# Performance work log

Measured on AMD Instinct MI355X. Metric: run time of the kernel, lower is better.

The kernel has to match this reference:

```python
import jax, jax.numpy as jnp
import numpy as np

B, T, D, H = 8, 1024, 1024, 16
DH = D // H
EPS = 1e-5


def setup_inputs() -> dict:
    key = jax.random.key(0)
    ks = jax.random.split(key, 8)
    s = 0.02
    return {
        "x": jax.random.normal(ks[0], (B, T, D), dtype=jnp.float32),
        # per-head Q/K/V weights stacked: (H, in_c, d_head), applied as x @ W
        "Wq": jax.random.normal(ks[1], (H, D, DH), dtype=jnp.float32) * s,
        "Wk": jax.random.normal(ks[2], (H, D, DH), dtype=jnp.float32) * s,
        "Wv": jax.random.normal(ks[3], (H, D, DH), dtype=jnp.float32) * s,
        # FFN weights stored (in, out): y = x @ W
        "W1": jax.random.normal(ks[4], (D, D), dtype=jnp.float32) * s,
        "W2": jax.random.normal(ks[5], (D, D), dtype=jnp.float32) * s,
        "g1": jnp.ones((D,), jnp.float32),
        "b1": jnp.zeros((D,), jnp.float32),
        "g2": jnp.ones((D,), jnp.float32),
        "b2": jnp.zeros((D,), jnp.float32),
    }


def _layer_norm(x, g, b):
    m = jnp.mean(x, axis=-1, keepdims=True)
    v = jnp.mean((x - m) ** 2, axis=-1, keepdims=True)  # biased, as torch LN
    return (x - m) * jax.lax.rsqrt(v + EPS) * g + b


def reference(x, Wq, Wk, Wv, W1, W2, g1, b1, g2, b2):
    b, t, d = x.shape
    dh = Wq.shape[-1]
    q = jnp.einsum("btc,hcd->bhtd", x, Wq)
    k = jnp.einsum("btc,hcd->bhtd", x, Wk)
    v = jnp.einsum("btc,hcd->bhtd", x, Wv)
    attn = jnp.einsum("bhtd,bhsd->bhts", q, k) / (dh ** 0.5)
    # Original: attn @ ones(T,T) -> every column equals rowsum(attn);
    # softmax(dim=1) over the query axis is then constant across columns,
    # so out[t] = softmax_t(rowsum)[t] * sum_s v[s]. Same math, reduced.
    rowsum = attn.sum(axis=-1)               # (B,H,T)
    p = jax.nn.softmax(rowsum, axis=-1)      # softmax over query index t
    vsum = v.sum(axis=2)                     # (B,H,DH)
    head_out = p[..., None] * vsum[:, :, None, :]        # (B,H,T,DH)
    out = head_out.transpose(0, 2, 1, 3).reshape(b, t, d)  # concat heads
    x1 = _layer_norm(x + out, g1, b1)
    ff = jax.nn.relu(x1 @ W1) @ W2           # dropout = identity (eval)
    return _layer_norm(x1 + ff, g2, b2)
```

## Files before the change

### kernel.cpp

```cpp
#include <hip/hip_runtime.h>

#define NB 8
#define NT 1024
#define ND 1024
#define NH 16
#define NDH 64
#define NM (NB*NT)
#define LNEPS 1e-5f

typedef __attribute__((ext_vector_type(8))) __bf16 bf16x8;
typedef __attribute__((ext_vector_type(4))) float f32x4;

__global__ void transpose_to_bf16(const float* __restrict__ W1, const float* __restrict__ W2,
                                  __bf16* __restrict__ WT1, __bf16* __restrict__ WT2) {
    __shared__ float tile[32][33];
    const float* W = blockIdx.z ? W2 : W1;
    __bf16* WT = blockIdx.z ? WT2 : WT1;
    int bx = blockIdx.x * 32;
    int by = blockIdx.y * 32;
    int tx = threadIdx.x;
    int ty = threadIdx.y;
    for (int i = ty; i < 32; i += 8)
        tile[i][tx] = W[(size_t)(by + i) * ND + bx + tx];
    __syncthreads();
    for (int i = ty; i < 32; i += 8)
        WT[(size_t)(bx + i) * ND + by + tx] = (__bf16)tile[tx][i];
}

__global__ void xsum_kernel(const float* __restrict__ x, float* __restrict__ xsum) {
    int b = blockIdx.x;
    int chunk = blockIdx.y;
    int tid = threadIdx.x;
    const float4* xp = (const float4*)(x + ((size_t)b * NT + chunk * 16) * ND) + tid;
    float4 s = {0.f, 0.f, 0.f, 0.f};
    #pragma unroll
    for (int t = 0; t < 16; ++t) {
        float4 v = xp[(size_t)t * (ND / 4)];
        s.x += v.x; s.y += v.y; s.z += v.z; s.w += v.w;
    }
    float* dst = xsum + b * ND + tid * 4;
    atomicAdd(dst + 0, s.x);
    atomicAdd(dst + 1, s.y);
    atomicAdd(dst + 2, s.z);
    atomicAdd(dst + 3, s.w);
}

__global__ void head_prep(const float* __restrict__ xsum,
                          const float* __restrict__ Wq, const float* __restrict__ Wk,
                          const float* __restrict__ Wv,
                          float* __restrict__ vsum, float* __restrict__ wqk) {
    int h = blockIdx.x, b = blockIdx.y;
    int t = threadIdx.x;
    int d = t & 63, q = t >> 6;
    __shared__ float part[2][4][NDH];
    __shared__ float ks[NDH];
    const float* xs = xsum + b * ND;
    float sk = 0.f, sv = 0.f;
    #pragma unroll 4
    for (int c = q * 256; c < q * 256 + 256; ++c) {
        float xv = xs[c];
        sk += xv * Wk[((size_t)h * ND + c) * NDH + d];
        sv += xv * Wv[((size_t)h * ND + c) * NDH + d];
    }
    part[0][q][d] = sk;
    part[1][q][d] = sv;
    __syncthreads();
    if (t < 64) {
        ks[t] = part[0][0][t] + part[0][1][t] + part[0][2][t] + part[0][3][t];
    } else if (t < 128) {
        int dd = t - 64;
        vsum[((size_t)b * NH + h) * NDH + dd] =
            part[1][0][dd] + part[1][1][dd] + part[1][2][dd] + part[1][3][dd];
    }
    __syncthreads();
    for (int c = t; c < ND; c += 256) {
        const float* wq = Wq + ((size_t)h * ND + c) * NDH;
        float s = 0.f;
        #pragma unroll 16
        for (int dd = 0; dd < NDH; ++dd) s += wq[dd] * ks[dd];
        wqk[((size_t)b * NH + h) * ND + c] = s * 0.125f;
    }
}

__global__ __launch_bounds__(256) void rowsum_kernel(const float* __restrict__ x,
                                                     const float* __restrict__ wqk,
                                                     float* __restrict__ rowsum) {
    int tc = blockIdx.x, b = blockIdx.y;
    int tid = threadIdx.x, wid = tid >> 6, lane = tid & 63;
    int t0 = tc * 16 + wid * 4;
    float acc[4][16];
    #pragma unroll
    for (int tq = 0; tq < 4; ++tq)
        #pragma unroll
        for (int h = 0; h < 16; ++h) acc[tq][h] = 0.f;
    const float4* wb = (const float4*)(wqk + (size_t)b * NH * ND);
    #pragma unroll
    for (int chunk = 0; chunk < 4; ++chunk) {
        float4 xv[4];
        #pragma unroll
        for (int tq = 0; tq < 4; ++tq)
            xv[tq] = ((const float4*)(x + ((size_t)b * NT + t0 + tq) * ND))[chunk * 64 + lane];
        #pragma unroll
        for (int h = 0; h < 16; ++h) {
            float4 wv = wb[h * 256 + chunk * 64 + lane];
            #pragma unroll
            for (int tq = 0; tq < 4; ++tq)
                acc[tq][h] += xv[tq].x * wv.x + xv[tq].y * wv.y +
                              xv[tq].z * wv.z + xv[tq].w * wv.w;
        }
    }
    bool c0 = lane & 1, c1 = lane & 2, c2 = lane & 4, c3 = lane & 8;
    float out4[4];
    #pragma unroll
    for (int tq = 0; tq < 4; ++tq) {
        float w8[8];
        #pragma unroll
        for (int j = 0; j < 8; ++j) {
            float send = c0 ? acc[tq][2 * j] : acc[tq][2 * j + 1];
            float recv = __shfl_xor(send, 1, 64);
            w8[j] = (c0 ? acc[tq][2 * j + 1] : acc[tq][2 * j]) + recv;
        }
        float u4[4];
        #pragma unroll
        for (int j = 0; j < 4; ++j) {
            float send = c1 ? w8[2 * j] : w8[2 * j + 1];
            float recv = __shfl_xor(send, 2, 64);
            u4[j] = (c1 ? w8[2 * j + 1] : w8[2 * j]) + recv;
        }
        float s2[2];
        #pragma unroll
        for (int j = 0; j < 2; ++j) {
            float send = c2 ? u4[2 * j] : u4[2 * j + 1];
            float recv = __shfl_xor(send, 4, 64);
            s2[j] = (c2 ? u4[2 * j + 1] : u4[2 * j]) + recv;
        }
        float send = c3 ? s2[0] : s2[1];
        float recv = __shfl_xor(send, 8, 64);
        float r = (c3 ? s2[1] : s2[0]) + recv;
        r += __shfl_xor(r, 16, 64);
        r += __shfl_xor(r, 32, 64);
        out4[tq] = r;
    }
    if (lane < 16) {
        float4 o = {out4[0], out4[1], out4[2], out4[3]};
        *(float4*)(rowsum + ((size_t)b * NH + lane) * NT + t0) = o;
    }
}

__global__ void softmax_kernel(float* __restrict__ rs) {
    int bh = blockIdx.x, tid = threadIdx.x;
    int wave = tid >> 6, lane = tid & 63;
    float* row = rs + (size_t)bh * NT;
    float4 v = ((float4*)row)[tid];
    float m = fmaxf(fmaxf(v.x, v.y), fmaxf(v.z, v.w));
    __shared__ float red[4];
    for (int off = 32; off; off >>= 1) m = fmaxf(m, __shfl_down(m, off, 64));
    if (lane == 0) red[wave] = m;
    __syncthreads();
    m = fmaxf(fmaxf(red[0], red[1]), fmaxf(red[2], red[3]));
    __syncthreads();
    float4 e;
    e.x = __expf(v.x - m); e.y = __expf(v.y - m);
    e.z = __expf(v.z - m); e.w = __expf(v.w - m);
    float s = e.x + e.y + e.z + e.w;
    for (int off = 32; off; off >>= 1) s += __shfl_down(s, off, 64);
    if (lane == 0) red[wave] = s;
    __syncthreads();
    s = red[0] + red[1] + red[2] + red[3];
    float inv = 1.f / s;
    e.x *= inv; e.y *= inv; e.z *= inv; e.w *= inv;
    ((float4*)row)[tid] = e;
}

__global__ void ln1_kernel(const float* __restrict__ x, const float* __restrict__ p,
                           const float* __restrict__ vsum,
                           const float* __restrict__ g1, const float* __restrict__ b1,
                           __bf16* __restrict__ x1b) {
    int t = blockIdx.x, b = blockIdx.y, tid = threadIdx.x;
    int wave = tid >> 6, lane = tid & 63;
    size_t rowoff = ((size_t)b * NT + t) * ND;
    float4 xv = ((const float4*)(x + rowoff))[tid];
    int h = tid >> 4;
    float pv = p[((size_t)b * NH + h) * NT + t];
    float4 vs = ((const float4*)(vsum + ((size_t)b * NH + h) * NDH))[tid & 15];
    float4 s;
    s.x = xv.x + pv * vs.x; s.y = xv.y + pv * vs.y;
    s.z = xv.z + pv * vs.z; s.w = xv.w + pv * vs.w;
    float sum = s.x + s.y + s.z + s.w;
    float sq = s.x * s.x + s.y * s.y + s.z * s.z + s.w * s.w;
    __shared__ float rs_[4], rq_[4];
    for (int off = 32; off; off >>= 1) {
        sum += __shfl_down(sum, off, 64);
        sq += __shfl_down(sq, off, 64);
    }
    if (lane == 0) { rs_[wave] = sum; rq_[wave] = sq; }
    __syncthreads();
    sum = rs_[0] + rs_[1] + rs_[2] + rs_[3];
    sq = rq_[0] + rq_[1] + rq_[2] + rq_[3];
    float mu = sum * (1.f / ND);
    float var = sq * (1.f / ND) - mu * mu;
    float rstd = rsqrtf(var + LNEPS);
    float4 g = ((const float4*)g1)[tid];
    float4 bb = ((const float4*)b1)[tid];
    union { __bf16 h4[4]; uint2 u; } pk;
    pk.h4[0] = (__bf16)((s.x - mu) * rstd * g.x + bb.x);
    pk.h4[1] = (__bf16)((s.y - mu) * rstd * g.y + bb.y);
    pk.h4[2] = (__bf16)((s.z - mu) * rstd * g.z + bb.z);
    pk.h4[3] = (__bf16)((s.w - mu) * rstd * g.w + bb.w);
    ((uint2*)(x1b + rowoff))[tid] = pk.u;
}

template <int RELU>
__global__ __launch_bounds__(256) void gemm_bf16(const __bf16* __restrict__ A,
                                                 const __bf16* __restrict__ BT,
                                                 __bf16* __restrict__ Cout) {
    const int K = 1024, N = 1024;
    __shared__ __bf16 As[128 * 64];
    __shared__ __bf16 Bs[128 * 64];
    int raw = blockIdx.x;
    int swz = (raw & 7) * 64 + (raw >> 3);
    int m0 = (swz >> 3) * 128;
    int n0 = (swz & 7) * 128;
    int tid = threadIdx.x;
    int wid = tid >> 6, lane = tid & 63;
    int wr = wid >> 1, wc = wid & 1;
    int r = lane & 15, g = lane >> 4;
    int srow = tid >> 3;
    int soff_e = (((tid & 7) * 16) ^ ((srow & 7) << 4)) >> 1;
    const __bf16* Ag = A + (size_t)(m0 + srow) * K + soff_e;
    const __bf16* Bg = BT + (size_t)(n0 + srow) * K + soff_e;
    int swz_r = (r & 7) << 4;
    f32x4 acc[4][4] = {};
    for (int k0 = 0; k0 < K; k0 += 64) {
        __syncthreads();
        #pragma unroll
        for (int j = 0; j < 4; ++j) {
            __builtin_amdgcn_global_load_lds(
                (const __attribute__((address_space(1))) unsigned int*)(Ag + (size_t)(j * 32) * K + k0),
                (__attribute__((address_space(3))) unsigned int*)&As[(j * 32 + wid * 8) * 64], 16, 0, 0);
            __builtin_amdgcn_global_load_lds(
                (const __attribute__((address_space(1))) unsigned int*)(Bg + (size_t)(j * 32) * K + k0),
                (__attribute__((address_space(3))) unsigned int*)&Bs[(j * 32 + wid * 8) * 64], 16, 0, 0);
        }
        __syncthreads();
        #pragma unroll
        for (int ks = 0; ks < 2; ++ks) {
            int ob = (ks * 64 + g * 16) ^ swz_r;
            bf16x8 af[4], bf[4];
            #pragma unroll
            for (int mf = 0; mf < 4; ++mf)
                af[mf] = *(const bf16x8*)((const char*)&As[(wr * 64 + mf * 16 + r) * 64] + ob);
            #pragma unroll
            for (int nf = 0; nf < 4; ++nf)
                bf[nf] = *(const bf16x8*)((const char*)&Bs[(wc * 64 + nf * 16 + r) * 64] + ob);
            #pragma unroll
            for (int mf = 0; mf < 4; ++mf)
                #pragma unroll
                for (int nf = 0; nf < 4; ++nf)
                    acc[mf][nf] = __builtin_amdgcn_mfma_f32_16x16x32_bf16(af[mf], bf[nf], acc[mf][nf], 0, 0, 0);
        }
    }
    #pragma unroll
    for (int mf = 0; mf < 4; ++mf) {
        #pragma unroll
        for (int nf = 0; nf < 4; ++nf) {
            int col = n0 + wc * 64 + nf * 16 + r;
            #pragma unroll
            for (int i = 0; i < 4; ++i) {
                int row = m0 + wr * 64 + mf * 16 + g * 4 + i;
                float v = acc[mf][nf][i];
                if (RELU) v = fmaxf(v, 0.f);
                Cout[(size_t)row * N + col] = (__bf16)v;
            }
        }
    }
}

__global__ void ln2_kernel(const __bf16* __restrict__ x1b, const __bf16* __restrict__ ffb,
                           float* __restrict__ out,
                           const float* __restrict__ g2, const float* __restrict__ b2) {
    int t = blockIdx.x, b = blockIdx.y, tid = threadIdx.x;
    int wave = tid >> 6, lane = tid & 63;
    size_t rowoff = ((size_t)b * NT + t) * ND;
    union { __bf16 h4[4]; uint2 u; } pk, pf;
    pk.u = ((const uint2*)(x1b + rowoff))[tid];
    pf.u = ((const uint2*)(ffb + rowoff))[tid];
    float4 s;
    s.x = (float)pk.h4[0] + (float)pf.h4[0];
    s.y = (float)pk.h4[1] + (float)pf.h4[1];
    s.z = (float)pk.h4[2] + (float)pf.h4[2];
    s.w = (float)pk.h4[3] + (float)pf.h4[3];
    float sum = s.x + s.y + s.z + s.w;
    float sq = s.x * s.x + s.y * s.y + s.z * s.z + s.w * s.w;
    __shared__ float rs_[4], rq_[4];
    for (int off = 32; off; off >>= 1) {
        sum += __shfl_down(sum, off, 64);
        sq += __shfl_down(sq, off, 64);
    }
    if (lane == 0) { rs_[wave] = sum; rq_[wave] = sq; }
    __syncthreads();
    sum = rs_[0] + rs_[1] + rs_[2] + rs_[3];
    sq = rq_[0] + rq_[1] + rq_[2] + rq_[3];
    float mu = sum * (1.f / ND);
    float var = sq * (1.f / ND) - mu * mu;
    float rstd = rsqrtf(var + LNEPS);
    float4 g = ((const float4*)g2)[tid];
    float4 bb = ((const float4*)b2)[tid];
    float4 o;
    o.x = (s.x - mu) * rstd * g.x + bb.x;
    o.y = (s.y - mu) * rstd * g.y + bb.y;
    o.z = (s.z - mu) * rstd * g.z + bb.z;
    o.w = (s.w - mu) * rstd * g.w + bb.w;
    ((float4*)(out + rowoff))[tid] = o;
}

extern "C" void kernel_launch(void* const* d_in, const int* in_sizes, int n_in,
                              void* d_out, int out_size, void* d_ws, size_t ws_size,
                              hipStream_t stream) {
    const float* x  = (const float*)d_in[0];
    const float* Wq = (const float*)d_in[1];
    const float* Wk = (const float*)d_in[2];
    const float* Wv = (const float*)d_in[3];
    const float* W1 = (const float*)d_in[4];
    const float* W2 = (const float*)d_in[5];
    const float* g1 = (const float*)d_in[6];
    const float* b1 = (const float*)d_in[7];
    const float* g2 = (const float*)d_in[8];
    const float* b2 = (const float*)d_in[9];
    float* out = (float*)d_out;

    char* w = (char*)d_ws;
    float* xsum = (float*)w;   w += (size_t)NB * ND * 4;
    float* vsum = (float*)w;   w += (size_t)NB * NH * NDH * 4;
    float* wqk  = (float*)w;   w += (size_t)NB * NH * ND * 4;
    float* rsum = (float*)w;   w += (size_t)NB * NH * NT * 4;
    __bf16* x1b = (__bf16*)w;  w += (size_t)NM * ND * 2;
    __bf16* h1b = (__bf16*)w;  w += (size_t)NM * ND * 2;
    __bf16* ffb = (__bf16*)w;  w += (size_t)NM * ND * 2;
    __bf16* w1t = (__bf16*)w;  w += (size_t)ND * ND * 2;
    __bf16* w2t = (__bf16*)w;  w += (size_t)ND * ND * 2;

    hipMemsetAsync(xsum, 0, (size_t)NB * ND * 4, stream);

    transpose_to_bf16<<<dim3(32, 32, 2), dim3(32, 8), 0, stream>>>(W1, W2, w1t, w2t);

    xsum_kernel<<<dim3(NB, 64), 256, 0, stream>>>(x, xsum);
    head_prep<<<dim3(NH, NB), 256, 0, stream>>>(xsum, Wq, Wk, Wv, vsum, wqk);
    rowsum_kernel<<<dim3(64, NB), 256, 0, stream>>>(x, wqk, rsum);
    softmax_kernel<<<NB * NH, 256, 0, stream>>>(rsum);
    ln1_kernel<<<dim3(NT, NB), 256, 0, stream>>>(x, rsum, vsum, g1, b1, x1b);

    gemm_bf16<1><<<512, 256, 0, stream>>>(x1b, w1t, h1b);
    gemm_bf16<0><<<512, 256, 0, stream>>>(h1b, w2t, ffb);
    ln2_kernel<<<dim3(NT, NB), 256, 0, stream>>>(x1b, ffb, out, g2, b2);
}
```

Before: 240.6 us.

## Split head_prep into batched K/V sum kernel and parallel Wq projection

Replaces the per-(head,batch) head_prep with a kernel that loads each Wk/Wv slice once and reuses it for all 8 batches, accumulating partial K/V sums across channel chunks with atomics. The Wq·ksum projection moves to its own kernel with more blocks and float4 loads. This cuts redundant weight traffic and raises parallelism, at the cost of one extra launch, a larger memset and atomic contention.

```diff
diff --git a/kernel.cpp b/kernel.cpp
--- a/kernel.cpp
+++ b/kernel.cpp
@@ -45,39 +45,71 @@
     atomicAdd(dst + 3, s.w);
 }
 
-__global__ void head_prep(const float* __restrict__ xsum,
-                          const float* __restrict__ Wq, const float* __restrict__ Wk,
-                          const float* __restrict__ Wv,
-                          float* __restrict__ vsum, float* __restrict__ wqk) {
-    int h = blockIdx.x, b = blockIdx.y;
+__global__ __launch_bounds__(256) void ksum_vsum_kernel(const float* __restrict__ xsum,
+                                                        const float* __restrict__ Wk,
+                                                        const float* __restrict__ Wv,
+                                                        float* __restrict__ ksumg,
+                                                        float* __restrict__ vsumg) {
+    int h = blockIdx.x, cs = blockIdx.y;
+    int t = threadIdx.x, lane = t & 63, w = t >> 6;
+    int c0 = cs * 64;
+    __shared__ float xs[8][64];
+    #pragma unroll
+    for (int i = 0; i < 2; ++i) {
+        int idx = t + i * 256;
+        xs[idx >> 6][idx & 63] = xsum[(idx >> 6) * ND + c0 + (idx & 63)];
+    }
+    __syncthreads();
+    float sk[8] = {}, sv[8] = {};
+    #pragma unroll 4
+    for (int j = 0; j < 16; ++j) {
+        int c = c0 + w * 16 + j;
+        float wk = Wk[((size_t)h * ND + c) * NDH + lane];
+        float wv = Wv[((size_t)h * ND + c) * NDH + lane];
+        #pragma unroll
+        for (int b = 0; b < 8; ++b) {
+            float xv = xs[b][w * 16 + j];
+            sk[b] += xv * wk;
+            sv[b] += xv * wv;
+        }
+    }
+    __shared__ float red[2][8][4][64];
+    #pragma unroll
+    for (int b = 0; b < 8; ++b) {
+        red[0][b][w][lane] = sk[b];
+        red[1][b][w][lane] = sv[b];
+    }
+    __syncthreads();
+    #pragma unroll
+    for (int i = 0; i < 4; ++i) {
+        int o = t + i * 256;
+        int d = o & 63, rest = o >> 6;
+        int a = rest >> 3, b = rest & 7;
+        float s = red[a][b][0][d] + red[a][b][1][d] + red[a][b][2][d] + red[a][b][3][d];
+        float* dst = a ? vsumg : ksumg;
+        atomicAdd(&dst[((size_t)b * NH + h) * NDH + d], s);
+    }
+}
+
+__global__ __launch_bounds__(256) void wqk_kernel(const float* __restrict__ ksumg,
+                                                  const float* __restrict__ Wq,
+                                                  float* __restrict__ wqk) {
+    int h = blockIdx.x, b = blockIdx.y, cs = blockIdx.z;
     int t = threadIdx.x;
-    int d = t & 63, q = t >> 6;
-    __shared__ float part[2][4][NDH];
     __shared__ float ks[NDH];
-    const float* xs = xsum + b * ND;
-    float sk = 0.f, sv = 0.f;
-    #pragma unroll 4
-    for (int c = q * 256; c < q * 256 + 256; ++c) {
-        float xv = xs[c];
-        sk += xv * Wk[((size_t)h * ND + c) * NDH + d];
-        sv += xv * Wv[((size_t)h * ND + c) * NDH + d];
-    }
-    part[0][q][d] = sk;
-    part[1][q][d] = sv;
-    __syncthreads();
-    if (t < 64) {
-        ks[t] = part[0][0][t] + part[0][1][t] + part[0][2][t] + part[0][3][t];
-    } else if (t < 128) {
-        int dd = t - 64;
-        vsum[((size_t)b * NH + h) * NDH + dd] =
-            part[1][0][dd] + part[1][1][dd] + part[1][2][dd] + part[1][3][dd];
-    }
-    __syncthreads();
-    for (int c = t; c < ND; c += 256) {
-        const float* wq = Wq + ((size_t)h * ND + c) * NDH;
+    if (t < 64) ks[t] = ksumg[((size_t)b * NH + h) * NDH + t];
+    __syncthreads();
+    #pragma unroll
+    for (int i = 0; i < 2; ++i) {
+        int c = cs * 512 + i * 256 + t;
+        const float4* wq = (const float4*)(Wq + ((size_t)h * ND + c) * NDH);
         float s = 0.f;
-        #pragma unroll 16
-        for (int dd = 0; dd < NDH; ++dd) s += wq[dd] * ks[dd];
+        #pragma unroll
+        for (int dq = 0; dq < 16; ++dq) {
+            float4 v = wq[dq];
+            s += v.x * ks[dq * 4] + v.y * ks[dq * 4 + 1] +
+                 v.z * ks[dq * 4 + 2] + v.w * ks[dq * 4 + 3];
+        }
         wqk[((size_t)b * NH + h) * ND + c] = s * 0.125f;
     }
 }
@@ -330,22 +362,24 @@
     float* out = (float*)d_out;
 
     char* w = (char*)d_ws;
-    float* xsum = (float*)w;   w += (size_t)NB * ND * 4;
-    float* vsum = (float*)w;   w += (size_t)NB * NH * NDH * 4;
-    float* wqk  = (float*)w;   w += (size_t)NB * NH * ND * 4;
-    float* rsum = (float*)w;   w += (size_t)NB * NH * NT * 4;
+    float* xsum  = (float*)w;  w += (size_t)NB * ND * 4;
+    float* ksumg = (float*)w;  w += (size_t)NB * NH * NDH * 4;
+    float* vsum  = (float*)w;  w += (size_t)NB * NH * NDH * 4;
+    float* wqk   = (float*)w;  w += (size_t)NB * NH * ND * 4;
+    float* rsum  = (float*)w;  w += (size_t)NB * NH * NT * 4;
     __bf16* x1b = (__bf16*)w;  w += (size_t)NM * ND * 2;
     __bf16* h1b = (__bf16*)w;  w += (size_t)NM * ND * 2;
     __bf16* ffb = (__bf16*)w;  w += (size_t)NM * ND * 2;
     __bf16* w1t = (__bf16*)w;  w += (size_t)ND * ND * 2;
     __bf16* w2t = (__bf16*)w;  w += (size_t)ND * ND * 2;
 
-    hipMemsetAsync(xsum, 0, (size_t)NB * ND * 4, stream);
+    hipMemsetAsync(xsum, 0, (size_t)(NB * ND + 2 * NB * NH * NDH) * 4, stream);
 
     transpose_to_bf16<<<dim3(32, 32, 2), dim3(32, 8), 0, stream>>>(W1, W2, w1t, w2t);
 
     xsum_kernel<<<dim3(NB, 64), 256, 0, stream>>>(x, xsum);
-    head_prep<<<dim3(NH, NB), 256, 0, stream>>>(xsum, Wq, Wk, Wv, vsum, wqk);
+    ksum_vsum_kernel<<<dim3(NH, 16), 256, 0, stream>>>(xsum, Wk, Wv, ksumg, vsum);
+    wqk_kernel<<<dim3(NH, NB, 2), 256, 0, stream>>>(ksumg, Wq, wqk);
     rowsum_kernel<<<dim3(64, NB), 256, 0, stream>>>(x, wqk, rsum);
     softmax_kernel<<<NB * NH, 256, 0, stream>>>(rsum);
     ln1_kernel<<<dim3(NT, NB), 256, 0, stream>>>(x, rsum, vsum, g1, b1, x1b);
```

Result: faster. 223.8 us (-7.0%).
